# Performance work log

Measured on AMD Instinct MI355X. Metric: run time of the kernel, lower is better.

## Reference

```python
import jax, jax.numpy as jnp
import numpy as np


def _lstm_layer(x, w_ih, w_hh, b_ih, b_hh):
    # x: [B, T, D]; PyTorch gate order: i, f, g, o. Returns [B, T, H].
    B, T, _ = x.shape
    H = w_hh.shape[1]
    # precompute input contribution once: [B, T, 4H]
    xg = jnp.einsum('btd,gd->btg', x, w_ih) + b_ih + b_hh
    xg = jnp.transpose(xg, (1, 0, 2))  # [T, B, 4H]

    def step(carry, xt):
        h, c = carry
        gates = xt + h @ w_hh.T
        i, f, g, o = jnp.split(gates, 4, axis=-1)
        i = jax.nn.sigmoid(i)
        f = jax.nn.sigmoid(f)
        g = jnp.tanh(g)
        o = jax.nn.sigmoid(o)
        c = f * c + i * g
        h = o * jnp.tanh(c)
        return (h, c), h

    h0 = jnp.zeros((B, H), dtype=x.dtype)
    c0 = jnp.zeros((B, H), dtype=x.dtype)
    _, hs = jax.lax.scan(step, (h0, c0), xg)
    return jnp.transpose(hs, (1, 0, 2))  # [B, T, H]


def setup_inputs() -> dict:
    key = jax.random.key(0)
    ks = jax.random.split(key, 16)
    B, T, D, H, V = 64, 512, 768, 256, 30522
    s_in = 1.0 / np.sqrt(H)
    def u(k, shape):
        return jax.random.uniform(k, shape, jnp.float32, -s_in, s_in)
    return {
        'x': jax.random.normal(ks[0], (B, T, D), jnp.float32),
        'w_ih0': u(ks[1], (4 * H, D)),
        'w_hh0': u(ks[2], (4 * H, H)),
        'b_ih0': u(ks[3], (4 * H,)),
        'b_hh0': u(ks[4], (4 * H,)),
        'w_ih1': u(ks[5], (4 * H, H)),
        'w_hh1': u(ks[6], (4 * H, H)),
        'b_ih1': u(ks[7], (4 * H,)),
        'b_hh1': u(ks[8], (4 * H,)),
        'ln_w': jnp.ones((H,), jnp.float32),
        'ln_b': jnp.zeros((H,), jnp.float32),
        'attn_w': u(ks[9], (1, H)),
        'fc_w': u(ks[10], (V, H)),
        'fc_b': u(ks[11], (V,)),
    }


def reference(x, w_ih0, w_hh0, b_ih0, b_hh0, w_ih1, w_hh1, b_ih1, b_hh1,
              ln_w, ln_b, attn_w, fc_w, fc_b):
    # two-layer LSTM (eval mode: no inter-layer dropout)
    h1 = _lstm_layer(x, w_ih0, w_hh0, b_ih0, b_hh0)
    h2 = _lstm_layer(h1, w_ih1, w_hh1, b_ih1, b_hh1)  # [B, T, H]
    # LayerNorm over last dim
    mu = jnp.mean(h2, axis=-1, keepdims=True)
    var = jnp.mean(jnp.square(h2 - mu), axis=-1, keepdims=True)
    normed = (h2 - mu) / jnp.sqrt(var + 1e-5) * ln_w + ln_b
    # attention pooling over seq dim
    scores = jnp.einsum('bth,oh->bto', normed, attn_w)  # [B, T, 1]
    w = jax.nn.softmax(scores, axis=1)
    attended = jnp.sum(w * normed, axis=1)  # [B, H]
    # final FC to vocab
    return attended @ fc_w.T + fc_b  # [B, V]
```

## Files before the change

kernel.cpp:

```cpp
#include <hip/hip_runtime.h>
#include <cstdint>

typedef _Float16 f16;
using f16x2 = __attribute__((ext_vector_type(2))) _Float16;
using f16x4 = __attribute__((ext_vector_type(4))) _Float16;
using f16x8 = __attribute__((ext_vector_type(8))) _Float16;
using f32x4 = __attribute__((ext_vector_type(4))) float;
using u32x4 = __attribute__((ext_vector_type(4))) uint32_t;
using i32x4 = __attribute__((ext_vector_type(4))) int;

#define GLB_PTR(p) ((const __attribute__((address_space(1))) void*)(p))
#define LDS_PTR(p) ((__attribute__((address_space(3))) void*)(p))

__device__ __forceinline__ float rcp_nr(float x) {
  float r = __builtin_amdgcn_rcpf(x);
  return fmaf(fmaf(-x, r, 1.0f), r, r);
}
__device__ __forceinline__ float sigmoidf_(float x) {
  float e = exp2f(-x * 1.44269504088896f);
  return rcp_nr(1.0f + e);
}
__device__ __forceinline__ float tanhf_(float x) {
  float e = exp2f(x * 2.88539008177793f);
  return 1.0f - 2.0f * rcp_nr(e + 1.0f);
}

__device__ __forceinline__ void mfma_i8(i32x4& d, u32x4 a, u32x4 b) {
  asm("v_mfma_i32_16x16x64_i8 %0, %1, %2, %0"
      : "+v"(d)
      : "v"(a), "a"(b));
}
__device__ __forceinline__ void mfma_i8_z(i32x4& d, u32x4 a, u32x4 b, const i32x4& zc) {
  asm("v_mfma_i32_16x16x64_i8 %0, %1, %2, %3"
      : "=v"(d)
      : "v"(a), "a"(b), "v"(zc));
}


__global__ void convert_all_kernel(const float* __restrict__ x, f16* __restrict__ x_h,
                                   const float* __restrict__ w0, f16* __restrict__ w0_h,
                                   const float* __restrict__ w1, f16* __restrict__ w1_h,
                                   const float* __restrict__ fw, f16* __restrict__ fw_h) {
  const long N0 = 6291456, N1 = N0 + 196608, N2 = N1 + 65536, N3 = N2 + 1953408;
  long stride = (long)gridDim.x * blockDim.x;
  for (long i = blockIdx.x * (long)blockDim.x + threadIdx.x; i < N3; i += stride) {
    const float* in; f16* out; long j;
    if (i < N0)      { in = x;  out = x_h;  j = i; }
    else if (i < N1) { in = w0; out = w0_h; j = i - N0; }
    else if (i < N2) { in = w1; out = w1_h; j = i - N1; }
    else             { in = fw; out = fw_h; j = i - N2; }
    f32x4 v = *(const f32x4*)(in + j * 4);
    f16x4 h;
    h[0] = (f16)v[0]; h[1] = (f16)v[1]; h[2] = (f16)v[2]; h[3] = (f16)v[3];
    *(f16x4*)(out + j * 4) = h;
  }
}

__global__ void addvec2_kernel(const float* __restrict__ a0, const float* __restrict__ b0,
                               float* __restrict__ o0,
                               const float* __restrict__ a1, const float* __restrict__ b1,
                               float* __restrict__ o1) {
  int i = blockIdx.x * blockDim.x + threadIdx.x;
  if (i < 1024) o0[i] = a0[i] + b0[i];
  else if (i < 2048) o1[i - 1024] = a1[i - 1024] + b1[i - 1024];
}

__global__ __launch_bounds__(256) void rowscale2_kernel(
    const float* __restrict__ whh0, float* __restrict__ qmul0, float* __restrict__ dmul0,
    const float* __restrict__ whh1, float* __restrict__ qmul1, float* __restrict__ dmul1) {
  int blk = blockIdx.x;
  const float* whh; float* qmul; float* dmul;
  if (blk < 16) { whh = whh0; qmul = qmul0; dmul = dmul0; }
  else          { whh = whh1; qmul = qmul1; dmul = dmul1; blk -= 16; }
  const int wv = (blk * 256 + (int)threadIdx.x) >> 6;
  const int lane = threadIdx.x & 63;
  for (int rr = 0; rr < 16; ++rr) {
    int r = wv * 16 + rr;
    f32x4 v = *(const f32x4*)(whh + r * 256 + lane * 4);
    float m = fmaxf(fmaxf(fabsf(v[0]), fabsf(v[1])), fmaxf(fabsf(v[2]), fabsf(v[3])));
#pragma unroll
    for (int s = 1; s < 64; s <<= 1) m = fmaxf(m, __shfl_xor(m, s, 64));
    if (lane == 0) {
      float sr = fmaxf(m, 1e-8f);
      qmul[r] = 127.0f / sr;
      dmul[r] = sr / 16129.0f;
    }
  }
}

__global__ void wq82_kernel(const float* __restrict__ whh0, const float* __restrict__ qmul0,
                            uint32_t* __restrict__ wq0,
                            const float* __restrict__ whh1, const float* __restrict__ qmul1,
                            uint32_t* __restrict__ wq1) {
  int i = blockIdx.x * blockDim.x + threadIdx.x;
  const float* whh; const float* qmul; uint32_t* wq;
  if (i < 65536) { whh = whh0; qmul = qmul0; wq = wq0; }
  else           { whh = whh1; qmul = qmul1; wq = wq1; i -= 65536; }
  int d = i & 3, l = (i >> 2) & 63, c = (i >> 8) & 3, t = i >> 10;
  int r = t * 16 + (l & 15);
  int k0 = c * 64 + ((l >> 4) & 3) * 16 + d * 4;
  float qm = qmul[r];
  uint32_t out = 0;
#pragma unroll
  for (int e = 0; e < 4; ++e) {
    int q = __float2int_rn(whh[r * 256 + k0 + e] * qm);
    q = min(127, max(-127, q));
    out |= ((uint32_t)(uint8_t)(int8_t)q) << (8 * e);
  }
  wq[i] = out;
}


template <int OUTF32>
__global__ __launch_bounds__(256) void gemm_bt_kernel(
    const f16* __restrict__ A, const f16* __restrict__ B,
    const float* __restrict__ bias, void* __restrict__ Cout,
    int M, int N, int K) {
  __shared__ __align__(16) f16 Al[128 * 32];
  __shared__ __align__(16) f16 Bl[128 * 32];
  const int tid = threadIdx.x;
  const int lane = tid & 63, wave = tid >> 6;
  const int bn = blockIdx.x, bm = blockIdx.y;
  const int qm = (wave >> 1) * 64, qn = (wave & 1) * 64;

  f32x4 acc[4][4];
#pragma unroll
  for (int i = 0; i < 4; ++i)
#pragma unroll
    for (int j = 0; j < 4; ++j) acc[i][j] = (f32x4){0.f, 0.f, 0.f, 0.f};

  const int c0 = tid, c1 = 256 + tid;
  const int row0 = c0 >> 2, off0 = c0 & 3;
  const int row1 = c1 >> 2, off1 = c1 & 3;
  const int gmA0 = min(bm * 128 + row0, M - 1);
  const int gmA1 = min(bm * 128 + row1, M - 1);
  const int gnB0 = min(bn * 128 + row0, N - 1);
  const int gnB1 = min(bn * 128 + row1, N - 1);

  f16* ldsA0 = &Al[(wave * 64) * 8];
  f16* ldsA1 = &Al[(256 + wave * 64) * 8];
  f16* ldsB0 = &Bl[(wave * 64) * 8];
  f16* ldsB1 = &Bl[(256 + wave * 64) * 8];

  for (int k0 = 0; k0 < K; k0 += 32) {
    __syncthreads();
    __builtin_amdgcn_global_load_lds(GLB_PTR(A + (size_t)gmA0 * K + k0 + off0 * 8),
                                     LDS_PTR(ldsA0), 16, 0, 0);
    __builtin_amdgcn_global_load_lds(GLB_PTR(A + (size_t)gmA1 * K + k0 + off1 * 8),
                                     LDS_PTR(ldsA1), 16, 0, 0);
    __builtin_amdgcn_global_load_lds(GLB_PTR(B + (size_t)gnB0 * K + k0 + off0 * 8),
                                     LDS_PTR(ldsB0), 16, 0, 0);
    __builtin_amdgcn_global_load_lds(GLB_PTR(B + (size_t)gnB1 * K + k0 + off1 * 8),
                                     LDS_PTR(ldsB1), 16, 0, 0);
    asm volatile("s_waitcnt vmcnt(0)" ::: "memory");
    __syncthreads();
    f16x8 af[4], bf[4];
#pragma unroll
    for (int mt = 0; mt < 4; ++mt)
      af[mt] = *(const f16x8*)&Al[(qm + mt * 16 + (lane & 15)) * 32 + (lane >> 4) * 8];
#pragma unroll
    for (int nt = 0; nt < 4; ++nt)
      bf[nt] = *(const f16x8*)&Bl[(qn + nt * 16 + (lane & 15)) * 32 + (lane >> 4) * 8];
#pragma unroll
    for (int mt = 0; mt < 4; ++mt)
#pragma unroll
      for (int nt = 0; nt < 4; ++nt)
        acc[mt][nt] = __builtin_amdgcn_mfma_f32_16x16x32_f16(af[mt], bf[nt], acc[mt][nt], 0, 0, 0);
  }

#pragma unroll
  for (int mt = 0; mt < 4; ++mt)
#pragma unroll
    for (int nt = 0; nt < 4; ++nt)
#pragma unroll
      for (int j = 0; j < 4; ++j) {
        int gm = bm * 128 + qm + mt * 16 + (lane >> 4) * 4 + j;
        int gn = bn * 128 + qn + nt * 16 + (lane & 15);
        if (gm < M && gn < N) {
          float v = acc[mt][nt][j] + bias[gn];
          if (OUTF32)
            ((float*)Cout)[(size_t)gm * N + gn] = v;
          else
            ((f16*)Cout)[(size_t)gm * N + gn] = (f16)v;
        }
      }
}


__global__ __launch_bounds__(512, 2) void lstm_rec_kernel(
    const f16* __restrict__ xg,
    const u32x4* __restrict__ wq,
    const float* __restrict__ dmul,
    f16* __restrict__ h_out,
    int T) {
  __shared__ __align__(16) uint8_t h8[2][512];
  const int b = blockIdx.x;
  const int tid = threadIdx.x;
  const int w = tid >> 6, lane = tid & 63;
  const int l15 = lane & 15, kg = (lane >> 4) & 3;
  const int base = w * 16 + l15;
  const int asel = ((l15 & 3) == 1) ? 256 : 0;
  const int sel = kg >> 1;
  const int u = base + sel * 128;

  u32x4 wt[8][4];
#pragma unroll
  for (int j = 0; j < 8; ++j)
#pragma unroll
    for (int c = 0; c < 4; ++c)
      wt[j][c] = wq[((w + 8 * j) * 4 + c) * 64 + lane];
  float sc[4], sc2[4];
#pragma unroll
  for (int j = 0; j < 4; ++j) {
    sc[j] = dmul[u + 256 * j];
    sc2[j] = sc[j] * (1.0f / 127.0f);
  }

  if (tid < 256) ((uint32_t*)h8)[tid] = 0;
  float cst = 0.f;
  __syncthreads();

  const f16* xt = xg + (size_t)b * T * 1024;
  f16* hob = h_out + (size_t)b * T * 256;

  f16 xc[4];
#pragma unroll
  for (int j = 0; j < 4; ++j) xc[j] = xt[u + 256 * j];

  const i32x4 zc = (i32x4){0, 0, 0, 0};

  for (int t = 0; t < T; ++t) {
    float xv[4];
#pragma unroll
    for (int j = 0; j < 4; ++j) xv[j] = (float)xc[j];
    const f16* xn = (t + 1 < T) ? xt + 1024 : xt;
#pragma unroll
    for (int j = 0; j < 4; ++j) xc[j] = xn[u + 256 * j];

    const uint8_t* hq = h8[t & 1] + asel;
    u32x4 afr0 = *(const u32x4*)(hq + 0 * 64 + kg * 16);
    i32x4 a0, a1, a2, a3, a4, a5, a6, a7;
    mfma_i8_z(a0, afr0, wt[0][0], zc);
    mfma_i8_z(a1, afr0, wt[1][0], zc);
    mfma_i8_z(a2, afr0, wt[2][0], zc);
    mfma_i8_z(a3, afr0, wt[3][0], zc);
    mfma_i8_z(a4, afr0, wt[4][0], zc);
    mfma_i8_z(a5, afr0, wt[5][0], zc);
    mfma_i8_z(a6, afr0, wt[6][0], zc);
    mfma_i8_z(a7, afr0, wt[7][0], zc);
#pragma unroll
    for (int c = 1; c < 4; ++c) {
      u32x4 afr = *(const u32x4*)(hq + c * 64 + kg * 16);
      mfma_i8(a0, afr, wt[0][c]);
      mfma_i8(a1, afr, wt[1][c]);
      mfma_i8(a2, afr, wt[2][c]);
      mfma_i8(a3, afr, wt[3][c]);
      mfma_i8(a4, afr, wt[4][c]);
      mfma_i8(a5, afr, wt[5][c]);
      mfma_i8(a6, afr, wt[6][c]);
      mfma_i8(a7, afr, wt[7][c]);
    }
    float dI0 = sel ? (float)a1[0] : (float)a0[0];
    float dI1 = sel ? (float)a1[1] : (float)a0[1];
    float dF0 = sel ? (float)a3[0] : (float)a2[0];
    float dF1 = sel ? (float)a3[1] : (float)a2[1];
    float dG0 = sel ? (float)a5[0] : (float)a4[0];
    float dG1 = sel ? (float)a5[1] : (float)a4[1];
    float dO0 = sel ? (float)a7[0] : (float)a6[0];
    float dO1 = sel ? (float)a7[1] : (float)a6[1];
    float gI = dI0 * sc[0] + dI1 * sc2[0] + xv[0];
    float gF = dF0 * sc[1] + dF1 * sc2[1] + xv[1];
    float gG = dG0 * sc[2] + dG1 * sc2[2] + xv[2];
    float gO = dO0 * sc[3] + dO1 * sc2[3] + xv[3];
    float iv = sigmoidf_(gI), fv = sigmoidf_(gF);
    float gv = tanhf_(gG),   ov = sigmoidf_(gO);
    cst = fv * cst + iv * gv;
    float hv = ov * tanhf_(cst);
    int hi = __float2int_rn(hv * 127.0f);
    int lo = __float2int_rn(fmaf((float)hi, -127.0f, hv * 16129.0f));
    uint8_t* hn = (uint8_t*)h8[(t + 1) & 1];
    if ((kg & 1) == 0) {
      hn[u] = (uint8_t)(int8_t)hi;
      hn[256 + u] = (uint8_t)(int8_t)lo;
      hob[(size_t)t * 256 + u] = (f16)hv;
    }
    xt += 1024;
    asm volatile("s_waitcnt lgkmcnt(0)" ::: "memory");
    __builtin_amdgcn_s_barrier();
    __builtin_amdgcn_sched_barrier(0);
  }
}


__global__ __launch_bounds__(256) void ln_attn_kernel(
    const f16* __restrict__ h2, const float* __restrict__ lnw,
    const float* __restrict__ lnb, const float* __restrict__ aw,
    f16* __restrict__ att_out) {
  const int b = blockIdx.x, tid = threadIdx.x;
  const int lane = tid & 63, wave = tid >> 6;
  __shared__ float smu[512], sis[512], ssc[512];
  __shared__ float vbuf[256];
  __shared__ float red[16];

  float vj = aw[tid] * lnw[tid];
  float uj = aw[tid] * lnb[tid];
  vbuf[tid] = vj;
  float rv = vj, ru = uj;
#pragma unroll
  for (int m = 1; m < 64; m <<= 1) { rv += __shfl_xor(rv, m, 64); ru += __shfl_xor(ru, m, 64); }
  if (lane == 0) { red[wave] = rv; red[4 + wave] = ru; }
  __syncthreads();
  const float Vsum = red[0] + red[1] + red[2] + red[3];
  const float Csum = red[4] + red[5] + red[6] + red[7];
  const f32x4 v4 = *(const f32x4*)&vbuf[lane * 4];
  const f16* hb = h2 + (size_t)b * 512 * 256;

  for (int tt = wave; tt < 512; tt += 4) {
    f16x4 hv = *(const f16x4*)(hb + (size_t)tt * 256 + lane * 4);
    float h0 = (float)hv[0], h1 = (float)hv[1], h2v = (float)hv[2], h3 = (float)hv[3];
    float s1 = h0 + h1 + h2v + h3;
    float s2 = h0 * h0 + h1 * h1 + h2v * h2v + h3 * h3;
    float sv = h0 * v4[0] + h1 * v4[1] + h2v * v4[2] + h3 * v4[3];
#pragma unroll
    for (int m = 1; m < 64; m <<= 1) {
      s1 += __shfl_xor(s1, m, 64);
      s2 += __shfl_xor(s2, m, 64);
      sv += __shfl_xor(sv, m, 64);
    }
    if (lane == 0) {
      float mu = s1 * (1.0f / 256.0f);
      float var = s2 * (1.0f / 256.0f) - mu * mu;
      float is = rsqrtf(var + 1e-5f);
      smu[tt] = mu; sis[tt] = is;
      ssc[tt] = (sv - mu * Vsum) * is + Csum;
    }
  }
  __syncthreads();
  float a0 = ssc[tid], a1 = ssc[tid + 256];
  float mx = fmaxf(a0, a1);
#pragma unroll
  for (int m = 1; m < 64; m <<= 1) mx = fmaxf(mx, __shfl_xor(mx, m, 64));
  if (lane == 0) red[wave] = mx;
  __syncthreads();
  mx = fmaxf(fmaxf(red[0], red[1]), fmaxf(red[2], red[3]));
  __syncthreads();
  float p0 = exp2f((a0 - mx) * 1.44269504f);
  float p1 = exp2f((a1 - mx) * 1.44269504f);
  float ps = p0 + p1;
  float pm = p0 * smu[tid] * sis[tid] + p1 * smu[tid + 256] * sis[tid + 256];
#pragma unroll
  for (int m = 1; m < 64; m <<= 1) { ps += __shfl_xor(ps, m, 64); pm += __shfl_xor(pm, m, 64); }
  if (lane == 0) { red[wave] = ps; red[8 + wave] = pm; }
  __syncthreads();
  const float S = red[0] + red[1] + red[2] + red[3];
  const float PM = (red[8] + red[9] + red[10] + red[11]) / S;
  ssc[tid] = p0 / S * sis[tid];
  ssc[tid + 256] = p1 / S * sis[tid + 256];
  __syncthreads();
  float acc = 0.f;
  for (int t = 0; t < 512; ++t) acc += ssc[t] * (float)hb[(size_t)t * 256 + tid];
  float att = lnw[tid] * (acc - PM) + lnb[tid];
  att_out[b * 256 + tid] = (f16)att;
}


extern "C" void kernel_launch(void* const* d_in, const int* in_sizes, int n_in,
                              void* d_out, int out_size, void* d_ws, size_t ws_size,
                              hipStream_t stream) {
  (void)in_sizes; (void)n_in; (void)out_size; (void)ws_size;
  const float* x    = (const float*)d_in[0];
  const float* wih0 = (const float*)d_in[1];
  const float* whh0 = (const float*)d_in[2];
  const float* bih0 = (const float*)d_in[3];
  const float* bhh0 = (const float*)d_in[4];
  const float* wih1 = (const float*)d_in[5];
  const float* whh1 = (const float*)d_in[6];
  const float* bih1 = (const float*)d_in[7];
  const float* bhh1 = (const float*)d_in[8];
  const float* lnw  = (const float*)d_in[9];
  const float* lnb  = (const float*)d_in[10];
  const float* aw   = (const float*)d_in[11];
  const float* fcw  = (const float*)d_in[12];
  const float* fcb  = (const float*)d_in[13];

  char* ws = (char*)d_ws;
  f16* x_h      = (f16*)(ws + 0);
  f16* h1       = (f16*)(ws + 0);
  f16* h2       = (f16*)(ws + 16777216);
  f16* wih0_h   = (f16*)(ws + 50331648);
  f16* wih1_h   = (f16*)(ws + 51904512);
  f16* fcw_h    = (f16*)(ws + 52428800);
  uint32_t* wq0 = (uint32_t*)(ws + 68056064);
  uint32_t* wq1 = (uint32_t*)(ws + 68318208);
  float* qmul0  = (float*)(ws + 68580352);
  float* dmul0  = (float*)(ws + 68584448);
  float* qmul1  = (float*)(ws + 68588544);
  float* dmul1  = (float*)(ws + 68592640);
  float* bsum0  = (float*)(ws + 69104640);
  float* bsum1  = (float*)(ws + 69108736);
  f16* att_h    = (f16*)(ws + 69112832);
  f16* xg       = (f16*)(ws + 69145600);

  convert_all_kernel<<<4096, 256, 0, stream>>>(x, x_h, wih0, wih0_h, wih1, wih1_h, fcw, fcw_h);
  addvec2_kernel<<<8, 256, 0, stream>>>(bih0, bhh0, bsum0, bih1, bhh1, bsum1);
  rowscale2_kernel<<<32, 256, 0, stream>>>(whh0, qmul0, dmul0, whh1, qmul1, dmul1);
  wq82_kernel<<<512, 256, 0, stream>>>(whh0, qmul0, wq0, whh1, qmul1, wq1);

  gemm_bt_kernel<0><<<dim3(8, 256), 256, 0, stream>>>(x_h, wih0_h, bsum0, xg, 32768, 1024, 768);
  lstm_rec_kernel<<<64, 512, 0, stream>>>(xg, (const u32x4*)wq0, dmul0, h1, 512);
  gemm_bt_kernel<0><<<dim3(8, 256), 256, 0, stream>>>(h1, wih1_h, bsum1, xg, 32768, 1024, 256);
  lstm_rec_kernel<<<64, 512, 0, stream>>>(xg, (const u32x4*)wq1, dmul1, h2, 512);
  ln_attn_kernel<<<64, 256, 0, stream>>>(h2, lnw, lnb, aw, att_h);
  gemm_bt_kernel<1><<<dim3(239, 1), 256, 0, stream>>>(att_h, fcw_h, fcb, d_out, 64, 30522, 256);
}
```

Baseline: 1.146 ms.

## Interleave gate columns in xg and swizzle GEMM block order

```diff
diff --git a/kernel.cpp b/kernel.cpp
--- a/kernel.cpp
+++ b/kernel.cpp
@@ -111,7 +111,7 @@
 }
 
 
-template <int OUTF32>
+template <int OUTF32, int PERM, int SWZ>
 __global__ __launch_bounds__(256) void gemm_bt_kernel(
     const f16* __restrict__ A, const f16* __restrict__ B,
     const float* __restrict__ bias, void* __restrict__ Cout,
@@ -120,7 +120,16 @@
   __shared__ __align__(16) f16 Bl[128 * 32];
   const int tid = threadIdx.x;
   const int lane = tid & 63, wave = tid >> 6;
-  const int bn = blockIdx.x, bm = blockIdx.y;
+  int bn, bm;
+  if (SWZ) {
+    int fid = blockIdx.y * gridDim.x + blockIdx.x;
+    int id2 = (fid & 7) * 256 + (fid >> 3);
+    bm = id2 >> 3;
+    bn = id2 & 7;
+  } else {
+    bn = blockIdx.x;
+    bm = blockIdx.y;
+  }
   const int qm = (wave >> 1) * 64, qn = (wave & 1) * 64;
 
   f32x4 acc[4][4];
@@ -178,10 +187,12 @@
         int gn = bn * 128 + qn + nt * 16 + (lane & 15);
         if (gm < M && gn < N) {
           float v = acc[mt][nt][j] + bias[gn];
-          if (OUTF32)
+          if (OUTF32) {
             ((float*)Cout)[(size_t)gm * N + gn] = v;
-          else
-            ((f16*)Cout)[(size_t)gm * N + gn] = (f16)v;
+          } else {
+            int col = PERM ? ((gn & 255) * 4 + (gn >> 8)) : gn;
+            ((f16*)Cout)[(size_t)gm * N + col] = (f16)v;
+          }
         }
       }
 }
@@ -223,19 +234,15 @@
   const f16* xt = xg + (size_t)b * T * 1024;
   f16* hob = h_out + (size_t)b * T * 256;
 
-  f16 xc[4];
-#pragma unroll
-  for (int j = 0; j < 4; ++j) xc[j] = xt[u + 256 * j];
+  f16x4 xc = *(const f16x4*)(xt + u * 4);
 
   const i32x4 zc = (i32x4){0, 0, 0, 0};
 
   for (int t = 0; t < T; ++t) {
-    float xv[4];
-#pragma unroll
-    for (int j = 0; j < 4; ++j) xv[j] = (float)xc[j];
+    float xv0 = (float)xc[0], xv1 = (float)xc[1];
+    float xv2 = (float)xc[2], xv3 = (float)xc[3];
     const f16* xn = (t + 1 < T) ? xt + 1024 : xt;
-#pragma unroll
-    for (int j = 0; j < 4; ++j) xc[j] = xn[u + 256 * j];
+    xc = *(const f16x4*)(xn + u * 4);
 
     const uint8_t* hq = h8[t & 1] + asel;
     u32x4 afr0 = *(const u32x4*)(hq + 0 * 64 + kg * 16);
@@ -268,10 +275,10 @@
     float dG1 = sel ? (float)a5[1] : (float)a4[1];
     float dO0 = sel ? (float)a7[0] : (float)a6[0];
     float dO1 = sel ? (float)a7[1] : (float)a6[1];
-    float gI = dI0 * sc[0] + dI1 * sc2[0] + xv[0];
-    float gF = dF0 * sc[1] + dF1 * sc2[1] + xv[1];
-    float gG = dG0 * sc[2] + dG1 * sc2[2] + xv[2];
-    float gO = dO0 * sc[3] + dO1 * sc2[3] + xv[3];
+    float gI = dI0 * sc[0] + dI1 * sc2[0] + xv0;
+    float gF = dF0 * sc[1] + dF1 * sc2[1] + xv1;
+    float gG = dG0 * sc[2] + dG1 * sc2[2] + xv2;
+    float gO = dO0 * sc[3] + dO1 * sc2[3] + xv3;
     float iv = sigmoidf_(gI), fv = sigmoidf_(gF);
     float gv = tanhf_(gG),   ov = sigmoidf_(gO);
     cst = fv * cst + iv * gv;
@@ -406,10 +413,10 @@
   rowscale2_kernel<<<32, 256, 0, stream>>>(whh0, qmul0, dmul0, whh1, qmul1, dmul1);
   wq82_kernel<<<512, 256, 0, stream>>>(whh0, qmul0, wq0, whh1, qmul1, wq1);
 
-  gemm_bt_kernel<0><<<dim3(8, 256), 256, 0, stream>>>(x_h, wih0_h, bsum0, xg, 32768, 1024, 768);
+  gemm_bt_kernel<0, 1, 1><<<dim3(8, 256), 256, 0, stream>>>(x_h, wih0_h, bsum0, xg, 32768, 1024, 768);
   lstm_rec_kernel<<<64, 512, 0, stream>>>(xg, (const u32x4*)wq0, dmul0, h1, 512);
-  gemm_bt_kernel<0><<<dim3(8, 256), 256, 0, stream>>>(h1, wih1_h, bsum1, xg, 32768, 1024, 256);
+  gemm_bt_kernel<0, 1, 1><<<dim3(8, 256), 256, 0, stream>>>(h1, wih1_h, bsum1, xg, 32768, 1024, 256);
   lstm_rec_kernel<<<64, 512, 0, stream>>>(xg, (const u32x4*)wq1, dmul1, h2, 512);
   ln_attn_kernel<<<64, 256, 0, stream>>>(h2, lnw, lnb, aw, att_h);
-  gemm_bt_kernel<1><<<dim3(239, 1), 256, 0, stream>>>(att_h, fcw_h, fcb, d_out, 64, 30522, 256);
-}
+  gemm_bt_kernel<1, 0, 0><<<dim3(239, 1), 256, 0, stream>>>(att_h, fcw_h, fcb, d_out, 64, 30522, 256);
+}
```

New measurement: 1.123 ms. -2.1%, faster.
